# Kernel tuning notes

Measured on AMD Instinct MI355X. Metric: run time of the kernel, lower is better.

The kernel has to match this reference:

```python
import jax, jax.numpy as jnp
import numpy as np

PI = float(np.pi)

def erp_xyz_coords(h, w):
    # matches calculate_erp_coord: pixel grid -> uv -> unit-sphere xyz
    yy, xx = jnp.meshgrid(jnp.linspace(0.0, h - 1.0, h), jnp.linspace(0.0, w - 1.0, w), indexing='ij')
    u = (xx - (w / 2.0 + 0.5)) / w * 2.0 * PI
    v = (yy - (h / 2.0 + 0.5)) / h * PI
    xyz = jnp.stack([jnp.cos(v) * jnp.sin(u), jnp.sin(v), jnp.cos(v) * jnp.cos(u)], axis=-1)
    return xyz.reshape(h * w, 3)  # (HW, 3)


def setup_inputs() -> dict:
    key = jax.random.key(0)
    ks = jax.random.split(key, 16)
    B, C, H, W = 1, 128, 16, 32
    Nkv = 1280
    s = 0.02
    inp = {
        'erp_feature': jax.random.normal(ks[0], (B, C, H, W), jnp.float32),
        'ico_feature': jax.random.normal(ks[1], (B, Nkv, C), jnp.float32),
        'ico_coord': jax.random.normal(ks[2], (B, Nkv, 3), jnp.float32),
        # SA branch params (torch Linear: y = x @ W.T + b, W is (out,in))
        'Wq_sa': jax.random.normal(ks[3], (C, C), jnp.float32) * s,
        'Wkv_sa': jax.random.normal(ks[4], (2 * C, C), jnp.float32) * s,
        'proj_sa_w': jax.random.normal(ks[5], (C, C), jnp.float32) * s,
        'proj_sa_b': jnp.zeros((C,), jnp.float32),
        # DA branch params
        'Wq_da': jax.random.normal(ks[6], (C, C), jnp.float32) * s,
        'Wkv_da': jax.random.normal(ks[7], (2 * C, C), jnp.float32) * s,
        'Wdelta': jax.random.normal(ks[8], (C, 3), jnp.float32) * s,
        'proj_da_w': jax.random.normal(ks[9], (C, C), jnp.float32) * s,
        'proj_da_b': jnp.zeros((C,), jnp.float32),
        # gates
        'gate_sa_w': jax.random.normal(ks[10], (C, 2 * C), jnp.float32) * s,
        'gate_da_w': jax.random.normal(ks[11], (C, 2 * C), jnp.float32) * s,
    }
    return inp


def _forward(erp_feature, ico_feature, ico_coord,
             Wq_sa, Wkv_sa, proj_sa_w, proj_sa_b,
             Wq_da, Wkv_da, Wdelta, proj_da_w, proj_da_b,
             gate_sa_w, gate_da_w):
    B, C, H, W = erp_feature.shape
    Nq = H * W
    q = erp_feature.reshape(B, C, Nq).transpose(0, 2, 1)  # (B, Nq, C)
    qc = erp_xyz_coords(H, W)[None]                        # (1, Nq, 3) broadcasts over B

    # ---- SA branch (iteration = 1) ----
    q_sa = q @ Wq_sa.T                                     # (B, Nq, C)
    kv_sa = (ico_feature @ Wkv_sa.T).reshape(B, -1, 2, C)
    k_sa, v_sa = kv_sa[:, :, 0], kv_sa[:, :, 1]
    attn_sa = jax.nn.softmax(jnp.einsum('bqc,bkc->bqk', q_sa, k_sa) * (C ** -0.5), axis=-1)
    out_sa = jnp.einsum('bqk,bkc->bqc', attn_sa, v_sa)
    # faithful to torch: .transpose(1,2).reshape(B, Nq, C) scrambles layout
    out_sa = out_sa.transpose(0, 2, 1).reshape(B, Nq, C)
    sa = out_sa @ proj_sa_w.T + proj_sa_b

    # ---- DA branch (iteration = 1) ----
    q_da = q @ Wq_da.T
    kv_da = (ico_feature @ Wkv_da.T).reshape(B, -1, 2, C)
    k_da, v_da = kv_da[:, :, 0], kv_da[:, :, 1]
    # feature affinity: sum_c exp(-|q_c - k_c|)   -> (B, Nq, Nkv)
    feat_aff = jnp.exp(-jnp.abs(q_da[:, :, None, :] - k_da[:, None, :, :])).sum(-1)
    # positional term: (exp(-|dq - dk|) @ Wdelta.T).sum(-1) == exp(...) . Wdelta.sum(0)
    pos_exp = jnp.exp(-jnp.abs(qc[:, :, None, :] - ico_coord[:, None, :, :]))  # (B,Nq,Nkv,3)
    pos_aff = jnp.einsum('bqkt,t->bqk', pos_exp, Wdelta.sum(0))
    attn_da = jax.nn.softmax((feat_aff + pos_aff) * (1.0 / C), axis=-1)
    out_da = jnp.einsum('bqk,bkc->bqc', attn_da, v_da)
    da = out_da @ proj_da_w.T + proj_da_b

    # ---- gated fusion ----
    cat = jnp.concatenate([sa, da], axis=-1)               # (B, Nq, 2C)
    sa_factor = jax.nn.sigmoid(cat @ gate_sa_w.T)
    da_factor = jax.nn.sigmoid(cat @ gate_da_w.T)
    fused = sa_factor * sa + da_factor * da                # (B, Nq, C)
    return fused.reshape(B, H, W, C).transpose(0, 3, 1, 2)  # (B, C, H, W)


def reference(erp_feature, ico_feature, ico_coord,
              Wq_sa, Wkv_sa, proj_sa_w, proj_sa_b,
              Wq_da, Wkv_da, Wdelta, proj_da_w, proj_da_b,
              gate_sa_w, gate_da_w):
    return _forward(erp_feature, ico_feature, ico_coord,
                    Wq_sa, Wkv_sa, proj_sa_w, proj_sa_b,
                    Wq_da, Wkv_da, Wdelta, proj_da_w, proj_da_b,
                    gate_sa_w, gate_da_w)
```

## Files before the change

### kernel.cpp

```cpp
#include <hip/hip_runtime.h>
#include <math.h>

#define NQ   512
#define NKV  1280
#define CDIM 128

#define OFF_WDSUM 0
#define OFF_SUMS  16
#define OFF_QSA   1056
#define OFF_QDA   66592
#define OFF_KSAT  132128
#define OFF_VSA   295968
#define OFF_KDAT  459808
#define OFF_VDA   623648
#define OFF_OUT   787488

__global__ __launch_bounds__(256) void prep_kernel(
    const float* __restrict__ erp, const float* __restrict__ ico,
    const float* __restrict__ wq_sa, const float* __restrict__ wq_da,
    const float* __restrict__ wkv_sa, const float* __restrict__ wkv_da,
    const float* __restrict__ wdelta, float* __restrict__ ws)
{
  int bx = blockIdx.x, t = threadIdx.x;
  if (bx < 320) {
    __shared__ float x4[4 * CDIM];
    int k0 = bx * 4;
    for (int i = t; i < 512; i += 256) {
      int ky = i >> 7, j = i & 127;
      x4[j * 4 + ky] = ico[(k0 + ky) * CDIM + j];
    }
    __syncthreads();
    const float4* wsa4 = (const float4*)(wkv_sa + t * CDIM);
    const float4* wda4 = (const float4*)(wkv_da + t * CDIM);
    float as0=0,as1=0,as2=0,as3=0, ad0=0,ad1=0,ad2=0,ad3=0;
    #pragma unroll 4
    for (int j4 = 0; j4 < 32; ++j4) {
      float4 wsv = wsa4[j4];
      float4 wdv = wda4[j4];
      float4 x0 = *(const float4*)&x4[(j4 * 4 + 0) * 4];
      float4 x1 = *(const float4*)&x4[(j4 * 4 + 1) * 4];
      float4 x2 = *(const float4*)&x4[(j4 * 4 + 2) * 4];
      float4 x3 = *(const float4*)&x4[(j4 * 4 + 3) * 4];
      as0 = fmaf(wsv.x, x0.x, as0); as1 = fmaf(wsv.x, x0.y, as1);
      as2 = fmaf(wsv.x, x0.z, as2); as3 = fmaf(wsv.x, x0.w, as3);
      ad0 = fmaf(wdv.x, x0.x, ad0); ad1 = fmaf(wdv.x, x0.y, ad1);
      ad2 = fmaf(wdv.x, x0.z, ad2); ad3 = fmaf(wdv.x, x0.w, ad3);
      as0 = fmaf(wsv.y, x1.x, as0); as1 = fmaf(wsv.y, x1.y, as1);
      as2 = fmaf(wsv.y, x1.z, as2); as3 = fmaf(wsv.y, x1.w, as3);
      ad0 = fmaf(wdv.y, x1.x, ad0); ad1 = fmaf(wdv.y, x1.y, ad1);
      ad2 = fmaf(wdv.y, x1.z, ad2); ad3 = fmaf(wdv.y, x1.w, ad3);
      as0 = fmaf(wsv.z, x2.x, as0); as1 = fmaf(wsv.z, x2.y, as1);
      as2 = fmaf(wsv.z, x2.z, as2); as3 = fmaf(wsv.z, x2.w, as3);
      ad0 = fmaf(wdv.z, x2.x, ad0); ad1 = fmaf(wdv.z, x2.y, ad1);
      ad2 = fmaf(wdv.z, x2.z, ad2); ad3 = fmaf(wdv.z, x2.w, ad3);
      as0 = fmaf(wsv.w, x3.x, as0); as1 = fmaf(wsv.w, x3.y, as1);
      as2 = fmaf(wsv.w, x3.z, as2); as3 = fmaf(wsv.w, x3.w, as3);
      ad0 = fmaf(wdv.w, x3.x, ad0); ad1 = fmaf(wdv.w, x3.y, ad1);
      ad2 = fmaf(wdv.w, x3.z, ad2); ad3 = fmaf(wdv.w, x3.w, ad3);
    }
    if (t < 128) {
      *(float4*)(ws + OFF_KSAT + t * NKV + k0) = make_float4(as0, as1, as2, as3);
      *(float4*)(ws + OFF_KDAT + t * NKV + k0) = make_float4(ad0, ad1, ad2, ad3);
    } else {
      int c = t - 128;
      ws[OFF_VSA + (k0 + 0) * CDIM + c] = as0;
      ws[OFF_VSA + (k0 + 1) * CDIM + c] = as1;
      ws[OFF_VSA + (k0 + 2) * CDIM + c] = as2;
      ws[OFF_VSA + (k0 + 3) * CDIM + c] = as3;
      ws[OFF_VDA + (k0 + 0) * CDIM + c] = ad0;
      ws[OFF_VDA + (k0 + 1) * CDIM + c] = ad1;
      ws[OFF_VDA + (k0 + 2) * CDIM + c] = ad2;
      ws[OFF_VDA + (k0 + 3) * CDIM + c] = ad3;
    }
  } else if (bx < 448) {
    __shared__ float q4[4 * CDIM];
    int n0 = (bx - 320) * 4;
    for (int i = t; i < 512; i += 256)
      q4[i] = erp[(i >> 2) * NQ + n0 + (i & 3)];
    __syncthreads();
    const float* w = (t < 128) ? wq_sa : wq_da;
    int c = t & 127;
    const float4* w4 = (const float4*)(w + c * CDIM);
    float a0 = 0.f, a1 = 0.f, a2 = 0.f, a3 = 0.f;
    #pragma unroll 8
    for (int j4 = 0; j4 < 32; ++j4) {
      float4 wv = w4[j4];
      float4 q0 = *(const float4*)&q4[(j4 * 4 + 0) * 4];
      float4 q1 = *(const float4*)&q4[(j4 * 4 + 1) * 4];
      float4 q2 = *(const float4*)&q4[(j4 * 4 + 2) * 4];
      float4 q3 = *(const float4*)&q4[(j4 * 4 + 3) * 4];
      a0 = fmaf(wv.x, q0.x, a0); a1 = fmaf(wv.x, q0.y, a1);
      a2 = fmaf(wv.x, q0.z, a2); a3 = fmaf(wv.x, q0.w, a3);
      a0 = fmaf(wv.y, q1.x, a0); a1 = fmaf(wv.y, q1.y, a1);
      a2 = fmaf(wv.y, q1.z, a2); a3 = fmaf(wv.y, q1.w, a3);
      a0 = fmaf(wv.z, q2.x, a0); a1 = fmaf(wv.z, q2.y, a1);
      a2 = fmaf(wv.z, q2.z, a2); a3 = fmaf(wv.z, q2.w, a3);
      a0 = fmaf(wv.w, q3.x, a0); a1 = fmaf(wv.w, q3.y, a1);
      a2 = fmaf(wv.w, q3.z, a2); a3 = fmaf(wv.w, q3.w, a3);
    }
    float* o = ws + ((t < 128) ? OFF_QSA : OFF_QDA);
    o[(n0 + 0) * CDIM + c] = a0;
    o[(n0 + 1) * CDIM + c] = a1;
    o[(n0 + 2) * CDIM + c] = a2;
    o[(n0 + 3) * CDIM + c] = a3;
  } else if (bx == 448) {
    *(float4*)(ws + OFF_SUMS + t * 4) = make_float4(0.f, 0.f, 0.f, 0.f);
    if (t < 3) {
      float s = 0.f;
      for (int i = 0; i < 128; ++i) s += wdelta[i * 3 + t];
      ws[OFF_WDSUM + t] = s;
    }
  } else {
    int base = OFF_OUT + (bx - 449) * 1024 + t * 4;
    *(float4*)(ws + base) = make_float4(0.f, 0.f, 0.f, 0.f);
  }
}

__global__ __launch_bounds__(256) void attn_kernel(
    const float* __restrict__ coord, float* __restrict__ ws)
{
  __shared__ __align__(16) float q2[CDIM * 2];
  __shared__ __align__(16) float se[2][256];
  __shared__ float red[4][2];
  __shared__ float part[2][2][CDIM];
  __shared__ float qcr[2][3];
  __shared__ float wdl[3];
  int t = threadIdx.x;
  int n0 = blockIdx.x * 2;
  int br = blockIdx.y;
  int z  = blockIdx.z;
  int k  = z * 256 + t;

  {
    int r = t >> 7, j = t & 127;
    const float* qsrc = ws + (br ? OFF_QDA : OFF_QSA);
    q2[j * 2 + r] = qsrc[(n0 + r) * CDIM + j];
  }
  if (br) {
    if (t < 2) {
      int n = n0 + t;
      float x = (float)(n & 31), y = (float)(n >> 5);
      float u  = (x - 16.5f) * 0.19634954084936207f;
      float vv = (y -  8.5f) * 0.19634954084936207f;
      float cv = cosf(vv);
      qcr[t][0] = cv * sinf(u);
      qcr[t][1] = sinf(vv);
      qcr[t][2] = cv * cosf(u);
    }
    if (t >= 64 && t < 67) wdl[t - 64] = ws[OFF_WDSUM + t - 64];
  }
  __syncthreads();

  float e0, e1;
  if (br == 0) {
    const float* kp = ws + OFF_KSAT + k;
    float a0 = 0.f, a1 = 0.f;
    #pragma unroll 8
    for (int j = 0; j < CDIM; ++j) {
      float kv = kp[j * NKV];
      float2 q = *(const float2*)&q2[j * 2];
      a0 = fmaf(q.x, kv, a0);
      a1 = fmaf(q.y, kv, a1);
    }
    const float scl = 0.088388347648318447f;
    e0 = __expf(a0 * scl);
    e1 = __expf(a1 * scl);
  } else {
    const float* kp = ws + OFF_KDAT + k;
    float a0 = 0.f, a1 = 0.f;
    #pragma unroll 8
    for (int j = 0; j < CDIM; ++j) {
      float kv = kp[j * NKV];
      float2 q = *(const float2*)&q2[j * 2];
      a0 += __expf(-fabsf(q.x - kv));
      a1 += __expf(-fabsf(q.y - kv));
    }
    float c0 = coord[k * 3], c1 = coord[k * 3 + 1], c2 = coord[k * 3 + 2];
    float w0 = wdl[0], w1 = wdl[1], w2 = wdl[2];
    float p0 = w0 * __expf(-fabsf(qcr[0][0] - c0))
             + w1 * __expf(-fabsf(qcr[0][1] - c1))
             + w2 * __expf(-fabsf(qcr[0][2] - c2));
    float p1 = w0 * __expf(-fabsf(qcr[1][0] - c0))
             + w1 * __expf(-fabsf(qcr[1][1] - c1))
             + w2 * __expf(-fabsf(qcr[1][2] - c2));
    const float i128 = 0.0078125f;
    e0 = __expf((a0 + p0) * i128);
    e1 = __expf((a1 + p1) * i128);
  }

  se[0][t] = e0; se[1][t] = e1;
  float s0 = e0, s1 = e1;
  #pragma unroll
  for (int o = 32; o > 0; o >>= 1) {
    s0 += __shfl_down(s0, o, 64);
    s1 += __shfl_down(s1, o, 64);
  }
  int lane = t & 63, wv = t >> 6;
  if (lane == 0) { red[wv][0] = s0; red[wv][1] = s1; }
  __syncthreads();
  if (t < 2)
    atomicAdd(ws + OFF_SUMS + br * 512 + n0 + t,
              red[0][t] + red[1][t] + red[2][t] + red[3][t]);

  const float* v = ws + (br ? OFF_VDA : OFF_VSA) + z * 256 * CDIM;
  int c = t & 127, h = t >> 7;
  const float* vp = v + h * 128 * CDIM + c;
  float acc0 = 0.f, acc1 = 0.f;
  #pragma unroll 2
  for (int ko = 0; ko < 128; ko += 4) {
    int kk = h * 128 + ko;
    float4 pa = *(const float4*)&se[0][kk];
    float4 pb = *(const float4*)&se[1][kk];
    float v0 = vp[(ko + 0) * CDIM];
    float v1 = vp[(ko + 1) * CDIM];
    float v2 = vp[(ko + 2) * CDIM];
    float v3 = vp[(ko + 3) * CDIM];
    acc0 = fmaf(pa.x, v0, acc0); acc1 = fmaf(pb.x, v0, acc1);
    acc0 = fmaf(pa.y, v1, acc0); acc1 = fmaf(pb.y, v1, acc1);
    acc0 = fmaf(pa.z, v2, acc0); acc1 = fmaf(pb.z, v2, acc1);
    acc0 = fmaf(pa.w, v3, acc0); acc1 = fmaf(pb.w, v3, acc1);
  }
  part[h][0][c] = acc0;
  part[h][1][c] = acc1;
  __syncthreads();
  {
    int r = t >> 7, cc = t & 127;
    float sum = part[0][r][cc] + part[1][r][cc];
    atomicAdd(ws + OFF_OUT + br * (NQ * CDIM) + (n0 + r) * CDIM + cc, sum);
  }
}

__global__ __launch_bounds__(256) void finalize_kernel(
    const float* __restrict__ psa, const float* __restrict__ bsa,
    const float* __restrict__ pda, const float* __restrict__ bda,
    const float* __restrict__ gsa, const float* __restrict__ gda,
    float* __restrict__ out, float* __restrict__ ws)
{
  __shared__ float sain[CDIM];
  __shared__ float dain[CDIM];
  __shared__ float cat[2 * CDIM];
  __shared__ float gl[2][CDIM];
  int i = blockIdx.x, t = threadIdx.x;
  int h = t >> 7, c = t & 127;
  if (h == 0) {
    int row = (i & 3) * 128 + c;
    float s = ws[OFF_SUMS + row];
    sain[c] = ws[OFF_OUT + row * CDIM + (i >> 2)] / s;
  } else {
    float s = ws[OFF_SUMS + 512 + i];
    dain[c] = ws[OFF_OUT + NQ * CDIM + i * CDIM + c] / s;
  }
  __syncthreads();
  {
    const float4* w4 = (const float4*)((h ? pda : psa) + c * CDIM);
    const float* in = h ? dain : sain;
    float a0 = 0, a1 = 0, a2 = 0, a3 = 0;
    #pragma unroll 8
    for (int j4 = 0; j4 < 32; ++j4) {
      float4 wv = w4[j4];
      float4 xv = *(const float4*)&in[j4 * 4];
      a0 = fmaf(wv.x, xv.x, a0); a1 = fmaf(wv.y, xv.y, a1);
      a2 = fmaf(wv.z, xv.z, a2); a3 = fmaf(wv.w, xv.w, a3);
    }
    cat[h * CDIM + c] = (h ? bda[c] : bsa[c]) + (a0 + a1) + (a2 + a3);
  }
  __syncthreads();
  {
    const float4* g4 = (const float4*)((h ? gda : gsa) + c * 2 * CDIM);
    float a0 = 0, a1 = 0, a2 = 0, a3 = 0;
    #pragma unroll 8
    for (int j4 = 0; j4 < 64; ++j4) {
      float4 gv = g4[j4];
      float4 cv = *(const float4*)&cat[j4 * 4];
      a0 = fmaf(gv.x, cv.x, a0); a1 = fmaf(gv.y, cv.y, a1);
      a2 = fmaf(gv.z, cv.z, a2); a3 = fmaf(gv.w, cv.w, a3);
    }
    gl[h][c] = 1.0f / (1.0f + __expf(-((a0 + a1) + (a2 + a3))));
  }
  __syncthreads();
  if (t < 128)
    out[t * NQ + i] = gl[0][t] * cat[t] + gl[1][t] * cat[CDIM + t];
}

extern "C" void kernel_launch(void* const* d_in, const int* in_sizes, int n_in,
                              void* d_out, int out_size, void* d_ws, size_t ws_size,
                              hipStream_t stream)
{
  (void)in_sizes; (void)n_in; (void)out_size; (void)ws_size;
  const float* erp       = (const float*)d_in[0];
  const float* ico       = (const float*)d_in[1];
  const float* coord     = (const float*)d_in[2];
  const float* wq_sa     = (const float*)d_in[3];
  const float* wkv_sa    = (const float*)d_in[4];
  const float* proj_sa_w = (const float*)d_in[5];
  const float* proj_sa_b = (const float*)d_in[6];
  const float* wq_da     = (const float*)d_in[7];
  const float* wkv_da    = (const float*)d_in[8];
  const float* wdelta    = (const float*)d_in[9];
  const float* proj_da_w = (const float*)d_in[10];
  const float* proj_da_b = (const float*)d_in[11];
  const float* gate_sa   = (const float*)d_in[12];
  const float* gate_da   = (const float*)d_in[13];
  float* out = (float*)d_out;
  float* ws  = (float*)d_ws;

  hipLaunchKernelGGL(prep_kernel, dim3(577), dim3(256), 0, stream,
                     erp, ico, wq_sa, wq_da, wkv_sa, wkv_da, wdelta, ws);
  hipLaunchKernelGGL(attn_kernel, dim3(256, 2, 5), dim3(256), 0, stream,
                     coord, ws);
  hipLaunchKernelGGL(finalize_kernel, dim3(512), dim3(256), 0, stream,
                     proj_sa_w, proj_sa_b, proj_da_w, proj_da_b,
                     gate_sa, gate_da, out, ws);
}
```

Before: 155.7 us.

## Retile attention to 4 queries per block and batch finalize two rows

The attention kernel now handles 4 query rows against 128 keys per block instead of 2 rows against 256 keys. The channel dimension is split across two thread halves, and partial scores are combined in shared memory, so each K load is reused across more queries. The grid is flattened with the DA branch blocks first, and the partial reduction for V is replaced by direct atomics per row. The finalize kernel processes two rows per block so each loaded weight is reused twice. The cost is extra syncs, half the threads idle during the softmax step, and twice as many output atomics.

New measurement: 142.8 us. 1.09x faster.

```diff
diff --git a/kernel.cpp b/kernel.cpp
--- a/kernel.cpp
+++ b/kernel.cpp
@@ -119,25 +119,26 @@
 __global__ __launch_bounds__(256) void attn_kernel(
     const float* __restrict__ coord, float* __restrict__ ws)
 {
-  __shared__ __align__(16) float q2[CDIM * 2];
-  __shared__ __align__(16) float se[2][256];
-  __shared__ float red[4][2];
-  __shared__ float part[2][2][CDIM];
-  __shared__ float qcr[2][3];
+  __shared__ __align__(16) float qjf[4 * CDIM];
+  __shared__ __align__(16) float psc[2][4][128];
+  __shared__ __align__(16) float posk[4][128];
+  __shared__ __align__(16) float se[4][128];
+  __shared__ float red[2][4];
+  __shared__ float qcr[4][3];
   __shared__ float wdl[3];
-  int t = threadIdx.x;
-  int n0 = blockIdx.x * 2;
-  int br = blockIdx.y;
-  int z  = blockIdx.z;
-  int k  = z * 256 + t;
-
-  {
-    int r = t >> 7, j = t & 127;
-    const float* qsrc = ws + (br ? OFF_QDA : OFF_QSA);
-    q2[j * 2 + r] = qsrc[(n0 + r) * CDIM + j];
+  int b = blockIdx.x, t = threadIdx.x;
+  int br = (b < 1280) ? 1 : 0;
+  int bb = br ? b : b - 1280;
+  int g = bb / 10, z = bb - g * 10;
+  int n0 = g * 4, k0 = z * 128;
+
+  const float* qsrc = ws + (br ? OFF_QDA : OFF_QSA);
+  for (int i = t; i < 512; i += 256) {
+    int r = i & 3, j = i >> 2;
+    qjf[j * 4 + r] = qsrc[(n0 + r) * CDIM + j];
   }
   if (br) {
-    if (t < 2) {
+    if (t < 4) {
       int n = n0 + t;
       float x = (float)(n & 31), y = (float)(n >> 5);
       float u  = (x - 16.5f) * 0.19634954084936207f;
@@ -151,66 +152,76 @@
   }
   __syncthreads();
 
-  float e0, e1;
-  if (br == 0) {
-    const float* kp = ws + OFF_KSAT + k;
-    float a0 = 0.f, a1 = 0.f;
-    #pragma unroll 8
-    for (int j = 0; j < CDIM; ++j) {
-      float kv = kp[j * NKV];
-      float2 q = *(const float2*)&q2[j * 2];
-      a0 = fmaf(q.x, kv, a0);
-      a1 = fmaf(q.y, kv, a1);
-    }
+  int kl = t & 127, jh = t >> 7;
+  int k = k0 + kl;
+  {
+    const float* kp = ws + (br ? OFF_KDAT : OFF_KSAT) + k + jh * 64 * NKV;
+    const float4* qj = (const float4*)&qjf[jh * 64 * 4];
+    float a0 = 0.f, a1 = 0.f, a2 = 0.f, a3 = 0.f;
+    if (br) {
+      #pragma unroll 4
+      for (int j = 0; j < 64; ++j) {
+        float kv = kp[j * NKV];
+        float4 q = qj[j];
+        a0 += __expf(-fabsf(q.x - kv)); a1 += __expf(-fabsf(q.y - kv));
+        a2 += __expf(-fabsf(q.z - kv)); a3 += __expf(-fabsf(q.w - kv));
+      }
+    } else {
+      #pragma unroll 8
+      for (int j = 0; j < 64; ++j) {
+        float kv = kp[j * NKV];
+        float4 q = qj[j];
+        a0 = fmaf(q.x, kv, a0); a1 = fmaf(q.y, kv, a1);
+        a2 = fmaf(q.z, kv, a2); a3 = fmaf(q.w, kv, a3);
+      }
+    }
+    psc[jh][0][kl] = a0; psc[jh][1][kl] = a1;
+    psc[jh][2][kl] = a2; psc[jh][3][kl] = a3;
+    if (br && jh == 1) {
+      float c0 = coord[k * 3], c1 = coord[k * 3 + 1], c2 = coord[k * 3 + 2];
+      float w0 = wdl[0], w1 = wdl[1], w2 = wdl[2];
+      #pragma unroll
+      for (int r = 0; r < 4; ++r)
+        posk[r][kl] = w0 * __expf(-fabsf(qcr[r][0] - c0))
+                    + w1 * __expf(-fabsf(qcr[r][1] - c1))
+                    + w2 * __expf(-fabsf(qcr[r][2] - c2));
+    }
+  }
+  __syncthreads();
+
+  if (t < 128) {
     const float scl = 0.088388347648318447f;
-    e0 = __expf(a0 * scl);
-    e1 = __expf(a1 * scl);
-  } else {
-    const float* kp = ws + OFF_KDAT + k;
-    float a0 = 0.f, a1 = 0.f;
-    #pragma unroll 8
-    for (int j = 0; j < CDIM; ++j) {
-      float kv = kp[j * NKV];
-      float2 q = *(const float2*)&q2[j * 2];
-      a0 += __expf(-fabsf(q.x - kv));
-      a1 += __expf(-fabsf(q.y - kv));
-    }
-    float c0 = coord[k * 3], c1 = coord[k * 3 + 1], c2 = coord[k * 3 + 2];
-    float w0 = wdl[0], w1 = wdl[1], w2 = wdl[2];
-    float p0 = w0 * __expf(-fabsf(qcr[0][0] - c0))
-             + w1 * __expf(-fabsf(qcr[0][1] - c1))
-             + w2 * __expf(-fabsf(qcr[0][2] - c2));
-    float p1 = w0 * __expf(-fabsf(qcr[1][0] - c0))
-             + w1 * __expf(-fabsf(qcr[1][1] - c1))
-             + w2 * __expf(-fabsf(qcr[1][2] - c2));
     const float i128 = 0.0078125f;
-    e0 = __expf((a0 + p0) * i128);
-    e1 = __expf((a1 + p1) * i128);
-  }
-
-  se[0][t] = e0; se[1][t] = e1;
-  float s0 = e0, s1 = e1;
-  #pragma unroll
-  for (int o = 32; o > 0; o >>= 1) {
-    s0 += __shfl_down(s0, o, 64);
-    s1 += __shfl_down(s1, o, 64);
-  }
-  int lane = t & 63, wv = t >> 6;
-  if (lane == 0) { red[wv][0] = s0; red[wv][1] = s1; }
-  __syncthreads();
-  if (t < 2)
-    atomicAdd(ws + OFF_SUMS + br * 512 + n0 + t,
-              red[0][t] + red[1][t] + red[2][t] + red[3][t]);
-
-  const float* v = ws + (br ? OFF_VDA : OFF_VSA) + z * 256 * CDIM;
+    float s[4];
+    #pragma unroll
+    for (int r = 0; r < 4; ++r) {
+      float tot = psc[0][r][t] + psc[1][r][t];
+      float l = br ? (tot + posk[r][t]) * i128 : tot * scl;
+      float e = __expf(l);
+      se[r][t] = e;
+      s[r] = e;
+    }
+    #pragma unroll
+    for (int o = 32; o > 0; o >>= 1) {
+      s[0] += __shfl_down(s[0], o, 64); s[1] += __shfl_down(s[1], o, 64);
+      s[2] += __shfl_down(s[2], o, 64); s[3] += __shfl_down(s[3], o, 64);
+    }
+    if ((t & 63) == 0) {
+      int w = t >> 6;
+      red[w][0] = s[0]; red[w][1] = s[1]; red[w][2] = s[2]; red[w][3] = s[3];
+    }
+  }
+  __syncthreads();
+  if (t < 4)
+    atomicAdd(ws + OFF_SUMS + br * 512 + n0 + t, red[0][t] + red[1][t]);
+
   int c = t & 127, h = t >> 7;
-  const float* vp = v + h * 128 * CDIM + c;
+  const float* vp = ws + (br ? OFF_VDA : OFF_VSA) + k0 * CDIM + c;
   float acc0 = 0.f, acc1 = 0.f;
-  #pragma unroll 2
+  #pragma unroll 4
   for (int ko = 0; ko < 128; ko += 4) {
-    int kk = h * 128 + ko;
-    float4 pa = *(const float4*)&se[0][kk];
-    float4 pb = *(const float4*)&se[1][kk];
+    float4 pa = *(const float4*)&se[h][ko];
+    float4 pb = *(const float4*)&se[h + 2][ko];
     float v0 = vp[(ko + 0) * CDIM];
     float v1 = vp[(ko + 1) * CDIM];
     float v2 = vp[(ko + 2) * CDIM];
@@ -220,14 +231,9 @@
     acc0 = fmaf(pa.z, v2, acc0); acc1 = fmaf(pb.z, v2, acc1);
     acc0 = fmaf(pa.w, v3, acc0); acc1 = fmaf(pb.w, v3, acc1);
   }
-  part[h][0][c] = acc0;
-  part[h][1][c] = acc1;
-  __syncthreads();
-  {
-    int r = t >> 7, cc = t & 127;
-    float sum = part[0][r][cc] + part[1][r][cc];
-    atomicAdd(ws + OFF_OUT + br * (NQ * CDIM) + (n0 + r) * CDIM + cc, sum);
-  }
+  float* op = ws + OFF_OUT + br * (NQ * CDIM);
+  atomicAdd(op + (n0 + h) * CDIM + c,     acc0);
+  atomicAdd(op + (n0 + h + 2) * CDIM + c, acc1);
 }
 
 __global__ __launch_bounds__(256) void finalize_kernel(
@@ -236,50 +242,66 @@
     const float* __restrict__ gsa, const float* __restrict__ gda,
     float* __restrict__ out, float* __restrict__ ws)
 {
-  __shared__ float sain[CDIM];
-  __shared__ float dain[CDIM];
-  __shared__ float cat[2 * CDIM];
-  __shared__ float gl[2][CDIM];
-  int i = blockIdx.x, t = threadIdx.x;
+  __shared__ float sain[2][CDIM];
+  __shared__ float dain[2][CDIM];
+  __shared__ float cat[2][2 * CDIM];
+  __shared__ float gl[2][2][CDIM];
+  int i0 = blockIdx.x * 2, t = threadIdx.x;
   int h = t >> 7, c = t & 127;
-  if (h == 0) {
-    int row = (i & 3) * 128 + c;
-    float s = ws[OFF_SUMS + row];
-    sain[c] = ws[OFF_OUT + row * CDIM + (i >> 2)] / s;
-  } else {
-    float s = ws[OFF_SUMS + 512 + i];
-    dain[c] = ws[OFF_OUT + NQ * CDIM + i * CDIM + c] / s;
+  #pragma unroll
+  for (int rr = 0; rr < 2; ++rr) {
+    int i = i0 + rr;
+    if (h == 0) {
+      int row = (i & 3) * 128 + c;
+      float s = ws[OFF_SUMS + row];
+      sain[rr][c] = ws[OFF_OUT + row * CDIM + (i >> 2)] / s;
+    } else {
+      float s = ws[OFF_SUMS + 512 + i];
+      dain[rr][c] = ws[OFF_OUT + NQ * CDIM + i * CDIM + c] / s;
+    }
   }
   __syncthreads();
   {
     const float4* w4 = (const float4*)((h ? pda : psa) + c * CDIM);
-    const float* in = h ? dain : sain;
-    float a0 = 0, a1 = 0, a2 = 0, a3 = 0;
+    const float* in0 = h ? dain[0] : sain[0];
+    const float* in1 = h ? dain[1] : sain[1];
+    float a0 = 0, a1 = 0, b0 = 0, b1 = 0;
     #pragma unroll 8
     for (int j4 = 0; j4 < 32; ++j4) {
       float4 wv = w4[j4];
-      float4 xv = *(const float4*)&in[j4 * 4];
-      a0 = fmaf(wv.x, xv.x, a0); a1 = fmaf(wv.y, xv.y, a1);
-      a2 = fmaf(wv.z, xv.z, a2); a3 = fmaf(wv.w, xv.w, a3);
-    }
-    cat[h * CDIM + c] = (h ? bda[c] : bsa[c]) + (a0 + a1) + (a2 + a3);
+      float4 x0 = *(const float4*)&in0[j4 * 4];
+      float4 x1 = *(const float4*)&in1[j4 * 4];
+      a0 = fmaf(wv.x, x0.x, a0); a1 = fmaf(wv.y, x0.y, a1);
+      a0 = fmaf(wv.z, x0.z, a0); a1 = fmaf(wv.w, x0.w, a1);
+      b0 = fmaf(wv.x, x1.x, b0); b1 = fmaf(wv.y, x1.y, b1);
+      b0 = fmaf(wv.z, x1.z, b0); b1 = fmaf(wv.w, x1.w, b1);
+    }
+    float bias = h ? bda[c] : bsa[c];
+    cat[0][h * CDIM + c] = bias + a0 + a1;
+    cat[1][h * CDIM + c] = bias + b0 + b1;
   }
   __syncthreads();
   {
     const float4* g4 = (const float4*)((h ? gda : gsa) + c * 2 * CDIM);
-    float a0 = 0, a1 = 0, a2 = 0, a3 = 0;
+    float a0 = 0, a1 = 0, b0 = 0, b1 = 0;
     #pragma unroll 8
     for (int j4 = 0; j4 < 64; ++j4) {
       float4 gv = g4[j4];
-      float4 cv = *(const float4*)&cat[j4 * 4];
-      a0 = fmaf(gv.x, cv.x, a0); a1 = fmaf(gv.y, cv.y, a1);
-      a2 = fmaf(gv.z, cv.z, a2); a3 = fmaf(gv.w, cv.w, a3);
-    }
-    gl[h][c] = 1.0f / (1.0f + __expf(-((a0 + a1) + (a2 + a3))));
-  }
-  __syncthreads();
-  if (t < 128)
-    out[t * NQ + i] = gl[0][t] * cat[t] + gl[1][t] * cat[CDIM + t];
+      float4 c0 = *(const float4*)&cat[0][j4 * 4];
+      float4 c1 = *(const float4*)&cat[1][j4 * 4];
+      a0 = fmaf(gv.x, c0.x, a0); a1 = fmaf(gv.y, c0.y, a1);
+      a0 = fmaf(gv.z, c0.z, a0); a1 = fmaf(gv.w, c0.w, a1);
+      b0 = fmaf(gv.x, c1.x, b0); b1 = fmaf(gv.y, c1.y, b1);
+      b0 = fmaf(gv.z, c1.z, b0); b1 = fmaf(gv.w, c1.w, b1);
+    }
+    gl[0][h][c] = 1.0f / (1.0f + __expf(-(a0 + a1)));
+    gl[1][h][c] = 1.0f / (1.0f + __expf(-(b0 + b1)));
+  }
+  __syncthreads();
+  {
+    int i = i0 + h;
+    out[c * NQ + i] = gl[h][0][c] * cat[h][c] + gl[h][1][c] * cat[h][CDIM + c];
+  }
 }
 
 extern "C" void kernel_launch(void* const* d_in, const int* in_sizes, int n_in,
@@ -306,9 +328,9 @@
 
   hipLaunchKernelGGL(prep_kernel, dim3(577), dim3(256), 0, stream,
                      erp, ico, wq_sa, wq_da, wkv_sa, wkv_da, wdelta, ws);
-  hipLaunchKernelGGL(attn_kernel, dim3(256, 2, 5), dim3(256), 0, stream,
+  hipLaunchKernelGGL(attn_kernel, dim3(2560), dim3(256), 0, stream,
                      coord, ws);
-  hipLaunchKernelGGL(finalize_kernel, dim3(512), dim3(256), 0, stream,
+  hipLaunchKernelGGL(finalize_kernel, dim3(256), dim3(256), 0, stream,
                      proj_sa_w, proj_sa_b, proj_da_w, proj_da_b,
                      gate_sa, gate_da, out, ws);
 }
```
